# Kernel tuning notes

Hardware: AMD Instinct MI355X
Metric: run time of the kernel (lower is better)

The kernel has to match this reference:

```python
import jax, jax.numpy as jnp
import numpy as np


def _dequantize(weight_q, scales, zeros, col_scale):
    # weight_q: [O, I_pad//2] int (nibble-packed), scales/zeros: [O, n_groups], col_scale: [I]
    O, half = weight_q.shape
    I_pad = half * 2
    n_g = scales.shape[1]
    gs = I_pad // n_g
    lo = (weight_q & 15).astype(scales.dtype)
    hi = (weight_q >> 4).astype(scales.dtype)
    # interleave: even columns = lo, odd columns = hi (matches q[:,0::2]/q[:,1::2] packing)
    q = jnp.stack([lo, hi], axis=-1).reshape(O, I_pad)
    q = q.reshape(O, n_g, gs)
    w = scales[:, :, None] * q + zeros[:, :, None]          # per-group affine dequant
    I = col_scale.shape[0]
    return w.reshape(O, I_pad)[:, :I] * col_scale[None, :]  # per-column AWQ scale


def setup_inputs() -> dict:
    key = jax.random.key(0)
    ks = jax.random.split(key, 6)
    B, S, I, O, n_g = 4, 2048, 4096, 11008, 64
    x = jax.random.normal(ks[0], (B, S, I), dtype=jnp.float32)
    weight_q = jax.random.randint(ks[1], (O, I // 2), 0, 256, dtype=jnp.int32)
    scales = jax.random.uniform(ks[2], (O, n_g), dtype=jnp.float32) * 0.02 + 1e-3
    zeros = jax.random.normal(ks[3], (O, n_g), dtype=jnp.float32) * 0.1
    col_scale = jax.random.uniform(ks[4], (I,), dtype=jnp.float32) * 1.5 + 0.25
    bias = jax.random.normal(ks[5], (O,), dtype=jnp.float32) * 0.01
    return {"x": x, "weight_q": weight_q, "scales": scales, "zeros": zeros,
            "col_scale": col_scale, "bias": bias}


def reference(x, weight_q, scales, zeros, col_scale, bias):
    w = _dequantize(weight_q, scales, zeros, col_scale).astype(x.dtype)  # [O, I]
    return jnp.einsum('bsi,oi->bso', x, w) + bias.astype(x.dtype)
```

## Files before the change

### kernel.cpp

```cpp
#include <hip/hip_runtime.h>
#include <cstdint>
#include <cstddef>

#define M_DIM 8192
#define N_DIM 11008
#define K_DIM 4096

typedef __attribute__((ext_vector_type(8))) __bf16 bf16x8;
typedef __attribute__((ext_vector_type(4))) float f32x4;
typedef __attribute__((ext_vector_type(8))) unsigned short ushort8v;

__device__ __forceinline__ unsigned short bf16rn(float f) {
  unsigned int u = __float_as_uint(f);
  u += 0x7FFFu + ((u >> 16) & 1u);
  return (unsigned short)(u >> 16);
}

__global__ void cvt_x_kernel(const float* __restrict__ x,
                             unsigned short* __restrict__ xb) {
  const int i = (blockIdx.x * 256 + threadIdx.x) * 8;
  const float4 a = *(const float4*)(x + i);
  const float4 b = *(const float4*)(x + i + 4);
  ushort8v o;
  o[0] = bf16rn(a.x); o[1] = bf16rn(a.y); o[2] = bf16rn(a.z); o[3] = bf16rn(a.w);
  o[4] = bf16rn(b.x); o[5] = bf16rn(b.y); o[6] = bf16rn(b.z); o[7] = bf16rn(b.w);
  *(ushort8v*)(xb + i) = o;
}

__global__ void dequant_w_kernel(const int* __restrict__ wq,
                                 const float* __restrict__ scales,
                                 const float* __restrict__ zeros,
                                 const float* __restrict__ csc,
                                 unsigned short* __restrict__ wb) {
  const int gid = blockIdx.x * 256 + threadIdx.x;
  const int row = gid >> 9;
  const int j4  = gid & 511;
  const int4 q = *(const int4*)(wq + row * 2048 + j4 * 4);
  const int g = j4 >> 3;
  const float s = scales[row * 64 + g];
  const float z = zeros[row * 64 + g];
  const int col = j4 * 8;
  const float4 c0 = *(const float4*)(csc + col);
  const float4 c1 = *(const float4*)(csc + col + 4);
  ushort8v o;
  o[0] = bf16rn((s * (float)( q.x        & 15) + z) * c0.x);
  o[1] = bf16rn((s * (float)((q.x >> 4)  & 15) + z) * c0.y);
  o[2] = bf16rn((s * (float)( q.y        & 15) + z) * c0.z);
  o[3] = bf16rn((s * (float)((q.y >> 4)  & 15) + z) * c0.w);
  o[4] = bf16rn((s * (float)( q.z        & 15) + z) * c1.x);
  o[5] = bf16rn((s * (float)((q.z >> 4)  & 15) + z) * c1.y);
  o[6] = bf16rn((s * (float)( q.w        & 15) + z) * c1.z);
  o[7] = bf16rn((s * (float)((q.w >> 4)  & 15) + z) * c1.w);
  *(ushort8v*)(wb + row * 4096 + col) = o;
}

__device__ __forceinline__ void gld_lds16(void* gp, void* lp) {
  __builtin_amdgcn_global_load_lds(
      (__attribute__((address_space(1))) void*)gp,
      (__attribute__((address_space(3))) void*)lp,
      16, 0, 0);
}

__global__ __launch_bounds__(256) void gemm_kernel(
    const unsigned short* __restrict__ A,
    const unsigned short* __restrict__ B,
    const float* __restrict__ bias,
    float* __restrict__ C) {
  __shared__ unsigned short As[128 * 32];
  __shared__ unsigned short Bs[128 * 32];

  const int tid  = threadIdx.x;
  const int lane = tid & 63;
  const int wave = tid >> 6;
  const int bm = blockIdx.y * 128;
  const int bn = blockIdx.x * 128;
  const int wm = (wave & 1) * 64;
  const int wn = (wave >> 1) * 64;

  f32x4 acc[4][4] = {};

  const int srow = wave * 32 + (lane >> 2);
  const int skol = (lane & 3) * 8;
  const unsigned short* gA0 = A + (size_t)(bm + srow) * K_DIM + skol;
  const unsigned short* gA1 = gA0 + 16 * K_DIM;
  const unsigned short* gB0 = B + (size_t)(bn + srow) * K_DIM + skol;
  const unsigned short* gB1 = gB0 + 16 * K_DIM;
  unsigned short* lA0 = &As[wave * 1024];
  unsigned short* lA1 = &As[wave * 1024 + 512];
  unsigned short* lB0 = &Bs[wave * 1024];
  unsigned short* lB1 = &Bs[wave * 1024 + 512];

  const int fr = lane & 15;
  const int fk = (lane >> 4) * 8;

  for (int kk = 0; kk < K_DIM; kk += 32) {
    gld_lds16((void*)(gA0 + kk), lA0);
    gld_lds16((void*)(gA1 + kk), lA1);
    gld_lds16((void*)(gB0 + kk), lB0);
    gld_lds16((void*)(gB1 + kk), lB1);
    __syncthreads();

    bf16x8 af[4], bfr[4];
#pragma unroll
    for (int i = 0; i < 4; ++i)
      af[i] = *(const bf16x8*)&As[(wm + i * 16 + fr) * 32 + fk];
#pragma unroll
    for (int j = 0; j < 4; ++j)
      bfr[j] = *(const bf16x8*)&Bs[(wn + j * 16 + fr) * 32 + fk];
#pragma unroll
    for (int i = 0; i < 4; ++i)
#pragma unroll
      for (int j = 0; j < 4; ++j)
        acc[i][j] = __builtin_amdgcn_mfma_f32_16x16x32_bf16(af[i], bfr[j],
                                                            acc[i][j], 0, 0, 0);
    __syncthreads();
  }

  const int col0 = bn + wn + fr;
  const int row0 = bm + wm + (lane >> 4) * 4;
#pragma unroll
  for (int j = 0; j < 4; ++j) {
    const float bv = bias[col0 + j * 16];
#pragma unroll
    for (int i = 0; i < 4; ++i) {
#pragma unroll
      for (int r = 0; r < 4; ++r) {
        C[(size_t)(row0 + i * 16 + r) * N_DIM + (col0 + j * 16)] =
            acc[i][j][r] + bv;
      }
    }
  }
}

extern "C" void kernel_launch(void* const* d_in, const int* in_sizes, int n_in,
                              void* d_out, int out_size, void* d_ws, size_t ws_size,
                              hipStream_t stream) {
  const float* x      = (const float*)d_in[0];
  const int*   wq     = (const int*)d_in[1];
  const float* scales = (const float*)d_in[2];
  const float* zeros  = (const float*)d_in[3];
  const float* csc    = (const float*)d_in[4];
  const float* bias   = (const float*)d_in[5];
  float* out = (float*)d_out;

  unsigned short* xb = (unsigned short*)d_ws;
  unsigned short* wb = (unsigned short*)((char*)d_ws + (size_t)M_DIM * K_DIM * 2);

  cvt_x_kernel<<<16384, 256, 0, stream>>>(x, xb);
  dequant_w_kernel<<<22016, 256, 0, stream>>>(wq, scales, zeros, csc, wb);
  dim3 grid(N_DIM / 128, M_DIM / 128);
  gemm_kernel<<<grid, 256, 0, stream>>>(xb, wb, bias, out);
}
```

Before: 1.448 ms.

## Rewrite GEMM as 256x256-tile, 8-wave, double-buffered pipelined kernel with swizzled LDS

Replaces the 128x128 single-buffered GEMM with a 256x256 tile computed by 8 waves. Global-to-LDS loads are staged two k-tiles ahead across eight interleaved phases with explicit vmcnt waits, barriers and setprio, so loads overlap MFMA work. LDS reads use an XOR swizzle to cut bank conflicts, and block indices are remapped for L2 locality. The kernel needs 128KB of dynamic LDS and more accumulator registers, and correctness depends on the hand-written wait counts.

```diff
diff --git a/kernel.cpp b/kernel.cpp
--- a/kernel.cpp
+++ b/kernel.cpp
@@ -5,6 +5,8 @@
 #define M_DIM 8192
 #define N_DIM 11008
 #define K_DIM 4096
+#define K_TILES 64
+#define NITER   32
 
 typedef __attribute__((ext_vector_type(8))) __bf16 bf16x8;
 typedef __attribute__((ext_vector_type(4))) float f32x4;
@@ -54,79 +56,136 @@
   *(ushort8v*)(wb + row * 4096 + col) = o;
 }
 
-__device__ __forceinline__ void gld_lds16(void* gp, void* lp) {
+
+__device__ __forceinline__ void gld_lds16(const void* gp, void* lp) {
   __builtin_amdgcn_global_load_lds(
       (__attribute__((address_space(1))) void*)gp,
       (__attribute__((address_space(3))) void*)lp,
       16, 0, 0);
 }
 
-__global__ __launch_bounds__(256) void gemm_kernel(
+#define BARRIER()    asm volatile("s_barrier" ::: "memory")
+#define WAIT_LGKM0() asm volatile("s_waitcnt lgkmcnt(0)" ::: "memory")
+#define WAIT_VM6()   asm volatile("s_waitcnt vmcnt(6)" ::: "memory")
+
+#define REGION(BUF, MAT, KH) (lds + ((((BUF) << 2) | ((MAT) << 1) | (KH)) << 13))
+
+#define STAGE(BUF, MAT, KH, KT)                                               \
+  {                                                                           \
+    const unsigned short* g_ =                                                \
+        ((MAT) == 0 ? Aps : Bps) + (size_t)(KT) * 64 + (KH) * 32;             \
+    unsigned short* l_ = REGION(BUF, MAT, KH) + wofs;                         \
+    gld_lds16((const void*)g_, (void*)l_);                                    \
+    gld_lds16((const void*)(g_ + rstep), (void*)(l_ + 4096));                 \
+  }
+
+#define PHASE(BUF, KS, MH, STAGE_CODE, DO_VM)                                 \
+  {                                                                           \
+    if ((MH) == 0) {                                                          \
+      const unsigned short* rb_ = REGION(BUF, 1, KS);                         \
+      bq[0] = *(const bf16x8*)(rb_ + boff[0]);                                \
+      bq[1] = *(const bf16x8*)(rb_ + boff[1]);                                \
+      bq[2] = *(const bf16x8*)(rb_ + boff[2]);                                \
+      bq[3] = *(const bf16x8*)(rb_ + boff[3]);                                \
+    }                                                                         \
+    {                                                                         \
+      const unsigned short* ra_ = REGION(BUF, 0, KS);                         \
+      aq[0] = *(const bf16x8*)(ra_ + aoff[MH][0]);                            \
+      aq[1] = *(const bf16x8*)(ra_ + aoff[MH][1]);                            \
+      aq[2] = *(const bf16x8*)(ra_ + aoff[MH][2]);                            \
+      aq[3] = *(const bf16x8*)(ra_ + aoff[MH][3]);                            \
+    }                                                                         \
+    STAGE_CODE;                                                               \
+    BARRIER();                                                                \
+    WAIT_LGKM0();                                                             \
+    __builtin_amdgcn_sched_barrier(0);                                        \
+    __builtin_amdgcn_s_setprio(1);                                            \
+    _Pragma("unroll")                                                         \
+    for (int j = 0; j < 4; ++j) {                                             \
+      _Pragma("unroll")                                                       \
+      for (int n = 0; n < 4; ++n) {                                           \
+        acc[(MH) * 4 + j][n] = __builtin_amdgcn_mfma_f32_16x16x32_bf16(       \
+            aq[j], bq[n], acc[(MH) * 4 + j][n], 0, 0, 0);                     \
+      }                                                                       \
+    }                                                                         \
+    __builtin_amdgcn_s_setprio(0);                                            \
+    if (DO_VM) { WAIT_VM6(); }                                                \
+    BARRIER();                                                                \
+  }
+
+__global__ __launch_bounds__(512, 2) void gemm_kernel(
     const unsigned short* __restrict__ A,
     const unsigned short* __restrict__ B,
     const float* __restrict__ bias,
     float* __restrict__ C) {
-  __shared__ unsigned short As[128 * 32];
-  __shared__ unsigned short Bs[128 * 32];
+  extern __shared__ unsigned short lds[];
 
   const int tid  = threadIdx.x;
   const int lane = tid & 63;
-  const int wave = tid >> 6;
-  const int bm = blockIdx.y * 128;
-  const int bn = blockIdx.x * 128;
-  const int wm = (wave & 1) * 64;
-  const int wn = (wave >> 1) * 64;
-
-  f32x4 acc[4][4] = {};
-
-  const int srow = wave * 32 + (lane >> 2);
-  const int skol = (lane & 3) * 8;
-  const unsigned short* gA0 = A + (size_t)(bm + srow) * K_DIM + skol;
-  const unsigned short* gA1 = gA0 + 16 * K_DIM;
-  const unsigned short* gB0 = B + (size_t)(bn + srow) * K_DIM + skol;
-  const unsigned short* gB1 = gB0 + 16 * K_DIM;
-  unsigned short* lA0 = &As[wave * 1024];
-  unsigned short* lA1 = &As[wave * 1024 + 512];
-  unsigned short* lB0 = &Bs[wave * 1024];
-  unsigned short* lB1 = &Bs[wave * 1024 + 512];
-
-  const int fr = lane & 15;
-  const int fk = (lane >> 4) * 8;
-
-  for (int kk = 0; kk < K_DIM; kk += 32) {
-    gld_lds16((void*)(gA0 + kk), lA0);
-    gld_lds16((void*)(gA1 + kk), lA1);
-    gld_lds16((void*)(gB0 + kk), lB0);
-    gld_lds16((void*)(gB1 + kk), lB1);
-    __syncthreads();
-
-    bf16x8 af[4], bfr[4];
-#pragma unroll
-    for (int i = 0; i < 4; ++i)
-      af[i] = *(const bf16x8*)&As[(wm + i * 16 + fr) * 32 + fk];
+  const int w    = tid >> 6;
+  const int wm   = w >> 2;
+  const int wn   = w & 3;
+
+  int flat = blockIdx.y * gridDim.x + blockIdx.x;
+  flat = (flat & 7) * 172 + (flat >> 3);
+  const int bn = (flat % 43) * 256;
+  const int bm = (flat / 43) * 256;
+
+  const int fr  = lane & 15;
+  const int kxu = ((lane >> 4) * 8) ^ (((fr >> 1) & 3) << 3);
+  int aoff[2][4], boff[4];
+#pragma unroll
+  for (int mh = 0; mh < 2; ++mh)
 #pragma unroll
     for (int j = 0; j < 4; ++j)
-      bfr[j] = *(const bf16x8*)&Bs[(wn + j * 16 + fr) * 32 + fk];
-#pragma unroll
-    for (int i = 0; i < 4; ++i)
-#pragma unroll
-      for (int j = 0; j < 4; ++j)
-        acc[i][j] = __builtin_amdgcn_mfma_f32_16x16x32_bf16(af[i], bfr[j],
-                                                            acc[i][j], 0, 0, 0);
-    __syncthreads();
-  }
-
-  const int col0 = bn + wn + fr;
-  const int row0 = bm + wm + (lane >> 4) * 4;
-#pragma unroll
-  for (int j = 0; j < 4; ++j) {
-    const float bv = bias[col0 + j * 16];
-#pragma unroll
-    for (int i = 0; i < 4; ++i) {
+      aoff[mh][j] = (wm * 128 + mh * 64 + j * 16 + fr) * 32 + kxu;
+#pragma unroll
+  for (int n = 0; n < 4; ++n)
+    boff[n] = (wn * 64 + n * 16 + fr) * 32 + kxu;
+
+  const int sl   = lane ^ ((lane >> 3) & 3);
+  const int skol = (sl & 3) * 8;
+  const unsigned short* Aps = A + (size_t)(bm + w * 16 + (sl >> 2)) * K_DIM + skol;
+  const unsigned short* Bps = B + (size_t)(bn + w * 16 + (sl >> 2)) * K_DIM + skol;
+  const size_t rstep = (size_t)128 * K_DIM;
+  const int wofs = w * 512;
+
+  f32x4 acc[8][4] = {};
+  bf16x8 aq[4], bq[4];
+
+  STAGE(0, 1, 0, 0); STAGE(0, 0, 0, 0); STAGE(0, 1, 1, 0); STAGE(0, 0, 1, 0);
+  STAGE(1, 1, 0, 1); STAGE(1, 0, 0, 1); STAGE(1, 1, 1, 1);
+  WAIT_VM6();
+  BARRIER();
+
+#pragma unroll 1
+  for (int i = 0; i < NITER; ++i) {
+    const int kt1 = 2 * i + 1;
+    const int kt2 = (2 * i + 2 < K_TILES) ? (2 * i + 2) : (K_TILES - 1);
+    const int kt3 = (2 * i + 3 < K_TILES) ? (2 * i + 3) : (K_TILES - 1);
+    PHASE(0, 0, 0, STAGE(1, 0, 1, kt1), 0);
+    PHASE(0, 0, 1, STAGE(0, 1, 0, kt2), 0);
+    PHASE(0, 1, 0, STAGE(0, 0, 0, kt2), 0);
+    PHASE(0, 1, 1, STAGE(0, 1, 1, kt2), 1);
+    PHASE(1, 0, 0, STAGE(0, 0, 1, kt2), 0);
+    PHASE(1, 0, 1, STAGE(1, 1, 0, kt3), 0);
+    PHASE(1, 1, 0, STAGE(1, 0, 0, kt3), 0);
+    PHASE(1, 1, 1, STAGE(1, 1, 1, kt3), 1);
+  }
+
+  const int orow = bm + wm * 128 + (lane >> 4) * 4;
+  const int ocol = bn + wn * 64 + fr;
+  float bv[4];
+#pragma unroll
+  for (int n = 0; n < 4; ++n) bv[n] = bias[ocol + n * 16];
+#pragma unroll
+  for (int mi = 0; mi < 8; ++mi) {
+    const int r0 = orow + (mi >> 2) * 64 + (mi & 3) * 16;
+#pragma unroll
+    for (int n = 0; n < 4; ++n) {
 #pragma unroll
       for (int r = 0; r < 4; ++r) {
-        C[(size_t)(row0 + i * 16 + r) * N_DIM + (col0 + j * 16)] =
-            acc[i][j][r] + bv;
+        C[(size_t)(r0 + r) * N_DIM + (ocol + n * 16)] = acc[mi][n][r] + bv[n];
       }
     }
   }
@@ -148,6 +207,13 @@
 
   cvt_x_kernel<<<16384, 256, 0, stream>>>(x, xb);
   dequant_w_kernel<<<22016, 256, 0, stream>>>(wq, scales, zeros, csc, wb);
-  dim3 grid(N_DIM / 128, M_DIM / 128);
-  gemm_kernel<<<grid, 256, 0, stream>>>(xb, wb, bias, out);
-}
+
+  static bool attr_set = false;
+  if (!attr_set) {
+    hipFuncSetAttribute(reinterpret_cast<const void*>(gemm_kernel),
+                        hipFuncAttributeMaxDynamicSharedMemorySize, 131072);
+    attr_set = true;
+  }
+  dim3 grid(N_DIM / 256, M_DIM / 256);
+  gemm_kernel<<<grid, 512, 131072, stream>>>(xb, wb, bias, out);
+}
```

New measurement: 1.168 ms. 1.24x faster.
